# Kernel optimization log

Hardware: AMD Instinct MI355X
Metric: run time of the kernel (lower is better)

Reference implementation:

```python
import jax, jax.numpy as jnp
import numpy as np

IMAGE_DIM = 224


def setup_inputs() -> dict:
    key = jax.random.key(0)
    k1, k2, k3, k4, k5 = jax.random.split(key, 5)
    N, H, W = 64, IMAGE_DIM, IMAGE_DIM
    im1 = jax.random.normal(k1, (N, 3, H, W), dtype=jnp.float32)
    im2 = jax.random.normal(k2, (N, 3, H, W), dtype=jnp.float32)
    C = jax.random.normal(k3, (N, 2, H, W), dtype=jnp.float32)
    M1 = jax.random.uniform(k4, (N, 1, H, W), dtype=jnp.float32)
    M2 = jax.random.uniform(k5, (N, 1, H, W), dtype=jnp.float32)
    return {"im1": im1, "im2": im2, "C": C, "M1": M1, "M2": M2}


def _grid(dtype):
    # q = [repeat(arange(H), W), tile(arange(W), H)], shape [2, H*W]
    x = jnp.repeat(jnp.arange(IMAGE_DIM), IMAGE_DIM)
    y = jnp.tile(jnp.arange(IMAGE_DIM), IMAGE_DIM)
    return jnp.stack([x, y]).astype(dtype)  # [2, HW]


def _bilinear_sample(imflat, qi):
    # imflat: [N, 3, HW], qi: [N, 2, HW] float coords
    HW = imflat.shape[-1]
    px, py = qi[:, 0], qi[:, 1]  # [N, HW]
    fx, cx = jnp.floor(px), jnp.ceil(px)
    fy, cy = jnp.floor(py), jnp.ceil(py)

    def gather_pixel(nx, ny):
        # weight = prod over axes of (1 - |point - neighbor|)
        w = (1.0 - jnp.abs(px - nx)) * (1.0 - jnp.abs(py - ny))  # [N, HW]
        ind = (nx + IMAGE_DIM * ny).astype(jnp.int32)
        ind = jnp.clip(ind, 0, HW - 1)  # guard against out-of-range neighbors
        pix = jnp.take_along_axis(imflat, ind[:, None, :], axis=2)  # [N, 3, HW]
        return w[:, None, :] * pix

    return (gather_pixel(fx, fy) + gather_pixel(cx, fy)
            + gather_pixel(fx, cy) + gather_pixel(cy * 0 + cx, cy))


def reference(im1, im2, C, M1, M2):
    N, ch, H, W = im1.shape
    HW = H * W
    q = _grid(im1.dtype)[None]              # [1, 2, HW]
    Cflat = C.reshape(N, 2, HW)
    a = _bilinear_sample(im1.reshape(N, ch, HW), q + Cflat).reshape(N, ch, H, W) * M1
    b = _bilinear_sample(im2.reshape(N, ch, HW), q - Cflat).reshape(N, ch, H, W) * M2
    return a + b
```

## Files before the change

kernel.cpp:

```cpp
#include <hip/hip_runtime.h>

#define IMG 224
#define HW (IMG * IMG)
#define TILE 32
#define PAD 4
#define REG (TILE + 2 * PAD)
#define RSA 41
#define TABA (REG * RSA)
#define RSB 44
#define TABB (REG * RSB)
#define BUFF 10080
#define TPT 7
#define NBLK 448
#define NXCD 8

typedef float vf2 __attribute__((ext_vector_type(2)));

struct U3 { float4 a, b, c; };

__device__ __forceinline__ U3 load3(const float* __restrict__ src, int gi) {
    U3 u;
    if (gi >= 0 && gi <= HW - 4) {
        u.a = *(const float4*)(src + gi);
        u.b = *(const float4*)(src + HW + gi);
        u.c = *(const float4*)(src + 2 * HW + gi);
    } else {
#pragma unroll
        for (int i = 0; i < 4; ++i) {
            int g = min(max(gi + i, 0), HW - 1);
            ((float*)&u.a)[i] = src[g];
            ((float*)&u.b)[i] = src[HW + g];
            ((float*)&u.c)[i] = src[2 * HW + g];
        }
    }
    return u;
}

__device__ __forceinline__ void writeU(float* __restrict__ base, int img,
                                       int r, int s, const U3& u) {
    float2* dA = (float2*)base + img * TABA + r * RSA + 4 * s;
    dA[0] = make_float2(u.a.x, u.b.x);
    dA[1] = make_float2(u.a.y, u.b.y);
    dA[2] = make_float2(u.a.z, u.b.z);
    dA[3] = make_float2(u.a.w, u.b.w);
    *(float4*)(base + 6560 + img * TABB + r * RSB + 4 * s) = u.c;
}

__device__ __forceinline__ void compute_px(
    const float* __restrict__ Bf, int xlo, int ylo,
    float xf, int p, int yfb,
    vf2 c0v, vf2 c1v, vf2 m1v, vf2 m2v,
    const float* __restrict__ i1n, const float* __restrict__ i2n,
    float* __restrict__ on)
{
    const float2* TA = (const float2*)Bf;
    const float*  TB = Bf + 6560;
    float acc0[2], acc1[2], acc2[2];

#pragma unroll
    for (int i = 0; i < 2; ++i) {
        const float yf  = (float)(yfb + i);
        const float cc0 = c0v[i], cc1 = c1v[i];
        const float m1i = m1v[i], m2i = m2v[i];
        float r0c, r1c, r2c;

        {
            float px = xf + cc0, py = yf + cc1;
            float fx = floorf(px), cx = ceilf(px);
            float fy = floorf(py), cy = ceilf(py);
            float wfx = 1.0f - (px - fx), wcx = 1.0f - (cx - px);
            float wfy = 1.0f - (py - fy), wcy = 1.0f - (cy - py);
            float w0 = wfx * wfy, w1 = wcx * wfy;
            float w2 = wfx * wcy, w3 = wcx * wcy;
            int gx0 = (int)fx, gy0 = (int)fy;
            int dx = (int)cx - gx0, dy = (int)cy - gy0;
            int q0 = gx0 - xlo, r0 = gy0 - ylo;
            int in = (q0 >= 0) & (q0 + dx <= REG - 1) &
                     (r0 >= 0) & (r0 + dy <= REG - 1);
            if (__all(in)) {
                int oA = r0 * RSA + q0, oB = r0 * RSB + q0;
                float2 A0 = TA[oA],            A1 = TA[oA + dx];
                float2 A2 = TA[oA + dy * RSA], A3 = TA[oA + dx + dy * RSA];
                float  b0 = TB[oB],            b1 = TB[oB + dx];
                float  b2 = TB[oB + dy * RSB], b3 = TB[oB + dx + dy * RSB];
                r0c = m1i * (w0 * A0.x + w1 * A1.x + w2 * A2.x + w3 * A3.x);
                r1c = m1i * (w0 * A0.y + w1 * A1.y + w2 * A2.y + w3 * A3.y);
                r2c = m1i * (w0 * b0   + w1 * b1   + w2 * b2   + w3 * b3);
            } else {
                int i0 = min(max(gx0      + IMG * gy0,        0), HW - 1);
                int i1 = min(max(gx0 + dx + IMG * gy0,        0), HW - 1);
                int i2 = min(max(gx0      + IMG * (gy0 + dy), 0), HW - 1);
                int i3 = min(max(gx0 + dx + IMG * (gy0 + dy), 0), HW - 1);
                r0c = m1i * (w0 * i1n[i0] + w1 * i1n[i1] +
                             w2 * i1n[i2] + w3 * i1n[i3]);
                r1c = m1i * (w0 * i1n[HW + i0] + w1 * i1n[HW + i1] +
                             w2 * i1n[HW + i2] + w3 * i1n[HW + i3]);
                r2c = m1i * (w0 * i1n[2 * HW + i0] + w1 * i1n[2 * HW + i1] +
                             w2 * i1n[2 * HW + i2] + w3 * i1n[2 * HW + i3]);
            }
        }
        {
            float px = xf - cc0, py = yf - cc1;
            float fx = floorf(px), cx = ceilf(px);
            float fy = floorf(py), cy = ceilf(py);
            float wfx = 1.0f - (px - fx), wcx = 1.0f - (cx - px);
            float wfy = 1.0f - (py - fy), wcy = 1.0f - (cy - py);
            float w0 = wfx * wfy, w1 = wcx * wfy;
            float w2 = wfx * wcy, w3 = wcx * wcy;
            int gx0 = (int)fx, gy0 = (int)fy;
            int dx = (int)cx - gx0, dy = (int)cy - gy0;
            int q0 = gx0 - xlo, r0 = gy0 - ylo;
            int in = (q0 >= 0) & (q0 + dx <= REG - 1) &
                     (r0 >= 0) & (r0 + dy <= REG - 1);
            if (__all(in)) {
                const float2* TA2 = TA + TABA;
                const float*  TB2 = TB + TABB;
                int oA = r0 * RSA + q0, oB = r0 * RSB + q0;
                float2 A0 = TA2[oA],            A1 = TA2[oA + dx];
                float2 A2 = TA2[oA + dy * RSA], A3 = TA2[oA + dx + dy * RSA];
                float  b0 = TB2[oB],            b1 = TB2[oB + dx];
                float  b2 = TB2[oB + dy * RSB], b3 = TB2[oB + dx + dy * RSB];
                r0c += m2i * (w0 * A0.x + w1 * A1.x + w2 * A2.x + w3 * A3.x);
                r1c += m2i * (w0 * A0.y + w1 * A1.y + w2 * A2.y + w3 * A3.y);
                r2c += m2i * (w0 * b0   + w1 * b1   + w2 * b2   + w3 * b3);
            } else {
                int i0 = min(max(gx0      + IMG * gy0,        0), HW - 1);
                int i1 = min(max(gx0 + dx + IMG * gy0,        0), HW - 1);
                int i2 = min(max(gx0      + IMG * (gy0 + dy), 0), HW - 1);
                int i3 = min(max(gx0 + dx + IMG * (gy0 + dy), 0), HW - 1);
                r0c += m2i * (w0 * i2n[i0] + w1 * i2n[i1] +
                              w2 * i2n[i2] + w3 * i2n[i3]);
                r1c += m2i * (w0 * i2n[HW + i0] + w1 * i2n[HW + i1] +
                              w2 * i2n[HW + i2] + w3 * i2n[HW + i3]);
                r2c += m2i * (w0 * i2n[2 * HW + i0] + w1 * i2n[2 * HW + i1] +
                              w2 * i2n[2 * HW + i2] + w3 * i2n[2 * HW + i3]);
            }
        }
        acc0[i] = r0c; acc1[i] = r1c; acc2[i] = r2c;
    }

    vf2 o0 = {acc0[0], acc0[1]};
    vf2 o1 = {acc1[0], acc1[1]};
    vf2 o2 = {acc2[0], acc2[1]};
    __builtin_nontemporal_store(o0, (vf2*)(on + p));
    __builtin_nontemporal_store(o1, (vf2*)(on + HW + p));
    __builtin_nontemporal_store(o2, (vf2*)(on + 2 * HW + p));
}

__global__ __launch_bounds__(512, 4) void vm_kernel(
    const float* __restrict__ im1, const float* __restrict__ im2,
    const float* __restrict__ C, const float* __restrict__ M1,
    const float* __restrict__ M2, float* __restrict__ out)
{
    __shared__ __align__(16) float lds[2 * BUFF];

    const int bid  = blockIdx.x;
    const int b    = (bid & (NXCD - 1)) * (NBLK / NXCD) + (bid >> 3);
    const int n    = b / 7;
    const int xcol = b - n * 7;

    const int x0  = xcol * TILE;
    const int t   = threadIdx.x;
    const int xlo = x0 - PAD;

    const float* i1n = im1 + (size_t)n * 3 * HW;
    const float* i2n = im2 + (size_t)n * 3 * HW;
    const float* Cn  = C  + (size_t)n * 2 * HW;
    const float* M1n = M1 + (size_t)n * HW;
    const float* M2n = M2 + (size_t)n * HW;
    float*       on  = out + (size_t)n * 3 * HW;

    const int tx    = t >> 4;
    const int ty0   = (t & 15) * 2;
    const int pbase = (x0 + tx) * IMG + ty0;
    const float xf  = (float)(x0 + tx);

    const bool a1 = (t < 400);
    const bool a2 = (t >= 112);
    const int e1 = t,        r1 = e1 / 10, s1 = e1 - 10 * r1;
    const int e2 = t - 112,  r2 = e2 / 10, s2 = e2 - 10 * r2;

    {
        int gb = xlo + IMG * (-PAD);
        U3 u1, u2;
        if (a1) u1 = load3(i1n, gb + IMG * r1 + 4 * s1);
        if (a2) u2 = load3(i2n, gb + IMG * r2 + 4 * s2);
        if (a1) writeU(lds, 0, r1, s1, u1);
        if (a2) writeU(lds, 1, r2, s2, u2);
    }
    vf2 c0c = __builtin_nontemporal_load((const vf2*)(Cn + pbase));
    vf2 c1c = __builtin_nontemporal_load((const vf2*)(Cn + HW + pbase));
    vf2 m1c = __builtin_nontemporal_load((const vf2*)(M1n + pbase));
    vf2 m2c = __builtin_nontemporal_load((const vf2*)(M2n + pbase));
    __syncthreads();

#pragma unroll 1
    for (int k = 0; k < TPT; ++k) {
        const int ylo = k * TILE - PAD;
        float* Bc = lds + (k & 1) * BUFF;
        float* Bn = lds + ((k + 1) & 1) * BUFF;

        U3 v1, v2;
        vf2 c0n, c1n, m1n, m2n;
        if (k < TPT - 1) {
            int gbn = xlo + IMG * (ylo + TILE);
            if (a1) v1 = load3(i1n, gbn + IMG * r1 + 4 * s1);
            if (a2) v2 = load3(i2n, gbn + IMG * r2 + 4 * s2);
            int pn = pbase + (k + 1) * TILE;
            c0n = __builtin_nontemporal_load((const vf2*)(Cn + pn));
            c1n = __builtin_nontemporal_load((const vf2*)(Cn + HW + pn));
            m1n = __builtin_nontemporal_load((const vf2*)(M1n + pn));
            m2n = __builtin_nontemporal_load((const vf2*)(M2n + pn));
        }

        compute_px(Bc, xlo, ylo, xf, pbase + k * TILE, k * TILE + ty0,
                   c0c, c1c, m1c, m2c, i1n, i2n, on);

        if (k < TPT - 1) {
            if (a1) writeU(Bn, 0, r1, s1, v1);
            if (a2) writeU(Bn, 1, r2, s2, v2);
            c0c = c0n; c1c = c1n; m1c = m1n; m2c = m2n;
        }
        __syncthreads();
    }
}

extern "C" void kernel_launch(void* const* d_in, const int* in_sizes, int n_in,
                              void* d_out, int out_size, void* d_ws, size_t ws_size,
                              hipStream_t stream) {
    const float* im1 = (const float*)d_in[0];
    const float* im2 = (const float*)d_in[1];
    const float* C   = (const float*)d_in[2];
    const float* M1  = (const float*)d_in[3];
    const float* M2  = (const float*)d_in[4];
    float* out = (float*)d_out;
    vm_kernel<<<dim3(NBLK), 512, 0, stream>>>(im1, im2, C, M1, M2, out);
}
```

Baseline: 176.8 us.

## Warp-specialize blocks into producer and consumer halves over flattened 2D tiles

Splits each 512-thread block into 256 compute threads, each handling four pixels with vf4 loads and stores, and 256 loader threads that prefetch the next tile's image halo into the double-buffered LDS. Tiles are now 32x32 squares taken from a flattened (image, tile) index, four per block, instead of seven tiles down one image column. The goal is to overlap global halo loads with the bilinear compute and to widen memory accesses. In exchange only half the threads do arithmetic, and a block's tiles can cross image boundaries, so the 4-pixel halo around each tile is reloaded instead of reused from a neighbouring tile.

```diff
diff --git a/kernel.cpp b/kernel.cpp
--- a/kernel.cpp
+++ b/kernel.cpp
@@ -4,17 +4,18 @@
 #define HW (IMG * IMG)
 #define TILE 32
 #define PAD 4
-#define REG (TILE + 2 * PAD)
+#define REG 40
 #define RSA 41
 #define TABA (REG * RSA)
 #define RSB 44
 #define TABB (REG * RSB)
 #define BUFF 10080
-#define TPT 7
-#define NBLK 448
+#define TPT 4
+#define NTILE (49 * 64)
+#define NBLK (NTILE / TPT)
 #define NXCD 8
 
-typedef float vf2 __attribute__((ext_vector_type(2)));
+typedef float vf4 __attribute__((ext_vector_type(4)));
 
 struct U3 { float4 a, b, c; };
 
@@ -46,20 +47,22 @@
     *(float4*)(base + 6560 + img * TABB + r * RSB + 4 * s) = u.c;
 }
 
-__device__ __forceinline__ void compute_px(
-    const float* __restrict__ Bf, int xlo, int ylo,
-    float xf, int p, int yfb,
-    vf2 c0v, vf2 c1v, vf2 m1v, vf2 m2v,
+__device__ __forceinline__ void compute_tile(
+    const float* __restrict__ Bf, int x0, int y0, int tx, int ty0,
+    vf4 c0v, vf4 c1v, vf4 m1v, vf4 m2v,
     const float* __restrict__ i1n, const float* __restrict__ i2n,
     float* __restrict__ on)
 {
     const float2* TA = (const float2*)Bf;
     const float*  TB = Bf + 6560;
-    float acc0[2], acc1[2], acc2[2];
+    const int xlo = x0 - PAD, ylo = y0 - PAD;
+    const int p  = (x0 + tx) * IMG + y0 + ty0;
+    const float xf = (float)(x0 + tx);
+    float acc0[4], acc1[4], acc2[4];
 
 #pragma unroll
-    for (int i = 0; i < 2; ++i) {
-        const float yf  = (float)(yfb + i);
+    for (int i = 0; i < 4; ++i) {
+        const float yf  = (float)(y0 + ty0 + i);
         const float cc0 = c0v[i], cc1 = c1v[i];
         const float m1i = m1v[i], m2i = m2v[i];
         float r0c, r1c, r2c;
@@ -139,12 +142,12 @@
         acc0[i] = r0c; acc1[i] = r1c; acc2[i] = r2c;
     }
 
-    vf2 o0 = {acc0[0], acc0[1]};
-    vf2 o1 = {acc1[0], acc1[1]};
-    vf2 o2 = {acc2[0], acc2[1]};
-    __builtin_nontemporal_store(o0, (vf2*)(on + p));
-    __builtin_nontemporal_store(o1, (vf2*)(on + HW + p));
-    __builtin_nontemporal_store(o2, (vf2*)(on + 2 * HW + p));
+    vf4 s0 = {acc0[0], acc0[1], acc0[2], acc0[3]};
+    vf4 s1 = {acc1[0], acc1[1], acc1[2], acc1[3]};
+    vf4 s2 = {acc2[0], acc2[1], acc2[2], acc2[3]};
+    __builtin_nontemporal_store(s0, (vf4*)(on + p));
+    __builtin_nontemporal_store(s1, (vf4*)(on + HW + p));
+    __builtin_nontemporal_store(s2, (vf4*)(on + 2 * HW + p));
 }
 
 __global__ __launch_bounds__(512, 4) void vm_kernel(
@@ -154,72 +157,97 @@
 {
     __shared__ __align__(16) float lds[2 * BUFF];
 
-    const int bid  = blockIdx.x;
-    const int b    = (bid & (NXCD - 1)) * (NBLK / NXCD) + (bid >> 3);
-    const int n    = b / 7;
-    const int xcol = b - n * 7;
-
-    const int x0  = xcol * TILE;
+    const int bid = blockIdx.x;
+    const int b   = (bid & (NXCD - 1)) * (NBLK / NXCD) + (bid >> 3);
+    const int g0  = b * TPT;
     const int t   = threadIdx.x;
-    const int xlo = x0 - PAD;
-
-    const float* i1n = im1 + (size_t)n * 3 * HW;
-    const float* i2n = im2 + (size_t)n * 3 * HW;
-    const float* Cn  = C  + (size_t)n * 2 * HW;
-    const float* M1n = M1 + (size_t)n * HW;
-    const float* M2n = M2 + (size_t)n * HW;
-    float*       on  = out + (size_t)n * 3 * HW;
-
-    const int tx    = t >> 4;
-    const int ty0   = (t & 15) * 2;
-    const int pbase = (x0 + tx) * IMG + ty0;
-    const float xf  = (float)(x0 + tx);
-
-    const bool a1 = (t < 400);
-    const bool a2 = (t >= 112);
-    const int e1 = t,        r1 = e1 / 10, s1 = e1 - 10 * r1;
-    const int e2 = t - 112,  r2 = e2 / 10, s2 = e2 - 10 * r2;
+
+    const int tx  = t >> 3;
+    const int ty0 = (t & 7) * 4;
+
+    int n0 = g0 / 49, tl0 = g0 - n0 * 49;
+    int x00 = (tl0 / 7) * TILE, y00 = (tl0 % 7) * TILE;
+
+    vf4 c0c, c1c, m1c, m2c;
+    if (t < 256) {
+        const float* Cn = C + (size_t)n0 * 2 * HW;
+        int p = (x00 + tx) * IMG + y00 + ty0;
+        c0c = __builtin_nontemporal_load((const vf4*)(Cn + p));
+        c1c = __builtin_nontemporal_load((const vf4*)(Cn + HW + p));
+        m1c = __builtin_nontemporal_load((const vf4*)(M1 + (size_t)n0 * HW + p));
+        m2c = __builtin_nontemporal_load((const vf4*)(M2 + (size_t)n0 * HW + p));
+    }
 
     {
-        int gb = xlo + IMG * (-PAD);
-        U3 u1, u2;
-        if (a1) u1 = load3(i1n, gb + IMG * r1 + 4 * s1);
-        if (a2) u2 = load3(i2n, gb + IMG * r2 + 4 * s2);
-        if (a1) writeU(lds, 0, r1, s1, u1);
-        if (a2) writeU(lds, 1, r2, s2, u2);
-    }
-    vf2 c0c = __builtin_nontemporal_load((const vf2*)(Cn + pbase));
-    vf2 c1c = __builtin_nontemporal_load((const vf2*)(Cn + HW + pbase));
-    vf2 m1c = __builtin_nontemporal_load((const vf2*)(M1n + pbase));
-    vf2 m2c = __builtin_nontemporal_load((const vf2*)(M2n + pbase));
+        const float* i1n = im1 + (size_t)n0 * 3 * HW;
+        const float* i2n = im2 + (size_t)n0 * 3 * HW;
+        int gb = (x00 - PAD) + IMG * (y00 - PAD);
+#pragma unroll
+        for (int kk = 0; kk < 2; ++kk) {
+            int e2 = t + 512 * kk;
+            if (e2 < 800) {
+                int img = (e2 >= 400);
+                int e = e2 - 400 * img;
+                int r = e / 10, s = e - 10 * r;
+                U3 u = load3(img ? i2n : i1n, gb + IMG * r + 4 * s);
+                writeU(lds, img, r, s, u);
+            }
+        }
+    }
     __syncthreads();
 
 #pragma unroll 1
     for (int k = 0; k < TPT; ++k) {
-        const int ylo = k * TILE - PAD;
-        float* Bc = lds + (k & 1) * BUFF;
-        float* Bn = lds + ((k + 1) & 1) * BUFF;
-
-        U3 v1, v2;
-        vf2 c0n, c1n, m1n, m2n;
-        if (k < TPT - 1) {
-            int gbn = xlo + IMG * (ylo + TILE);
-            if (a1) v1 = load3(i1n, gbn + IMG * r1 + 4 * s1);
-            if (a2) v2 = load3(i2n, gbn + IMG * r2 + 4 * s2);
-            int pn = pbase + (k + 1) * TILE;
-            c0n = __builtin_nontemporal_load((const vf2*)(Cn + pn));
-            c1n = __builtin_nontemporal_load((const vf2*)(Cn + HW + pn));
-            m1n = __builtin_nontemporal_load((const vf2*)(M1n + pn));
-            m2n = __builtin_nontemporal_load((const vf2*)(M2n + pn));
-        }
-
-        compute_px(Bc, xlo, ylo, xf, pbase + k * TILE, k * TILE + ty0,
-                   c0c, c1c, m1c, m2c, i1n, i2n, on);
-
-        if (k < TPT - 1) {
-            if (a1) writeU(Bn, 0, r1, s1, v1);
-            if (a2) writeU(Bn, 1, r2, s2, v2);
-            c0c = c0n; c1c = c1n; m1c = m1n; m2c = m2n;
+        float* bufC = lds + (k & 1) * BUFF;
+        float* bufN = lds + ((k + 1) & 1) * BUFF;
+        int gk = g0 + k;
+        int nk = gk / 49, tlk = gk - nk * 49;
+        int x0 = (tlk / 7) * TILE, y0 = (tlk % 7) * TILE;
+
+        if (t < 256) {
+            vf4 c0n, c1n, m1n, m2n;
+            if (k + 1 < TPT) {
+                int gn = gk + 1;
+                int nn = gn / 49, tln = gn - nn * 49;
+                int xn = (tln / 7) * TILE, yn = (tln % 7) * TILE;
+                const float* Cn = C + (size_t)nn * 2 * HW;
+                int pn = (xn + tx) * IMG + yn + ty0;
+                c0n = __builtin_nontemporal_load((const vf4*)(Cn + pn));
+                c1n = __builtin_nontemporal_load((const vf4*)(Cn + HW + pn));
+                m1n = __builtin_nontemporal_load((const vf4*)(M1 + (size_t)nn * HW + pn));
+                m2n = __builtin_nontemporal_load((const vf4*)(M2 + (size_t)nn * HW + pn));
+            }
+            const float* i1n = im1 + (size_t)nk * 3 * HW;
+            const float* i2n = im2 + (size_t)nk * 3 * HW;
+            compute_tile(bufC, x0, y0, tx, ty0, c0c, c1c, m1c, m2c,
+                         i1n, i2n, out + (size_t)nk * 3 * HW);
+            if (k + 1 < TPT) { c0c = c0n; c1c = c1n; m1c = m1n; m2c = m2n; }
+        } else {
+            if (k + 1 < TPT) {
+                int gn = gk + 1;
+                int nn = gn / 49, tln = gn - nn * 49;
+                int xn = (tln / 7) * TILE, yn = (tln % 7) * TILE;
+                const float* i1n = im1 + (size_t)nn * 3 * HW;
+                const float* i2n = im2 + (size_t)nn * 3 * HW;
+                int gb = (xn - PAD) + IMG * (yn - PAD);
+                int u = t - 256;
+                int r1 = u / 10, s1 = u - 10 * r1;
+                int r2 = (u + 256) / 10, s2 = (u + 256) - 10 * r2;
+                bool h2 = (u < 144);
+                U3 a1 = load3(i1n, gb + IMG * r1 + 4 * s1);
+                U3 b1 = load3(i2n, gb + IMG * r1 + 4 * s1);
+                U3 a2, b2;
+                if (h2) {
+                    a2 = load3(i1n, gb + IMG * r2 + 4 * s2);
+                    b2 = load3(i2n, gb + IMG * r2 + 4 * s2);
+                }
+                writeU(bufN, 0, r1, s1, a1);
+                writeU(bufN, 1, r1, s1, b1);
+                if (h2) {
+                    writeU(bufN, 0, r2, s2, a2);
+                    writeU(bufN, 1, r2, s2, b2);
+                }
+            }
         }
         __syncthreads();
     }
```

Result: slower. 199.4 us (+12.8%).
